# Kernel optimization log

Measured on AMD Instinct MI355X. Metric: run time of the kernel, lower is better.

The kernel has to match this reference:

```python
import math
import jax, jax.numpy as jnp
import numpy as np

D_MODEL = 1024
N_HEADS = 16


def setup_inputs() -> dict:
    key = jax.random.key(0)
    ks = jax.random.split(key, 5)
    B, S, D = 4, 2048, D_MODEL
    std = math.sqrt(2.0 / (D + D))
    x = jax.random.normal(ks[0], (B, S, D), dtype=jnp.float32)
    wq = jax.random.normal(ks[1], (D, D), dtype=jnp.float32) * std
    wk = jax.random.normal(ks[2], (D, D), dtype=jnp.float32) * std
    wv = jax.random.normal(ks[3], (D, D), dtype=jnp.float32) * std
    wo = jax.random.normal(ks[4], (D, D), dtype=jnp.float32) * std
    return {"x": x, "wq": wq, "wk": wk, "wv": wv, "wo": wo}


def reference(x, wq, wk, wv, wo):
    B, S, D = x.shape
    H = N_HEADS
    dk = D // H
    # projections: weight is (d_out, d_in) -> y_...j = x_...i W_ji
    def proj(w):
        y = jnp.einsum('bsi,ji->bsj', x, w)
        return y.reshape(B, S, H, dk).transpose(0, 2, 1, 3)  # b h s dk
    Q, K, V = proj(wq), proj(wk), proj(wv)
    scores = jnp.einsum('bhnd,bhmd->bhnm', Q, K) / math.sqrt(dk)
    causal = jnp.tril(jnp.ones((S, S), dtype=bool))  # True = attend
    scores = jnp.where(causal, scores, -jnp.inf)
    weights = jax.nn.softmax(scores, axis=-1)
    attn = jnp.einsum('bhnm,bhmd->bhnd', weights, V)
    attn = attn.transpose(0, 2, 1, 3).reshape(B, S, D)
    return jnp.einsum('bsi,ji->bsj', attn, wo)
```

## Files before the change

### kernel.cpp

```cpp
#include <hip/hip_runtime.h>
#include <hip/hip_bf16.h>
#include <cstdint>

#define D_MODEL 1024
#define NHEADS  16
#define DK      64
#define BATCH   4
#define SEQ     2048
#define MROWS   (BATCH * SEQ)
#define NQT2    (SEQ / 128)

#define QSCALE 0.18033688011112042f

typedef __attribute__((ext_vector_type(4))) float  f32x4;
typedef __attribute__((ext_vector_type(8))) __bf16 bf16x8;
typedef __attribute__((ext_vector_type(8))) short  short8;

__device__ __forceinline__ unsigned short f2bf(float f) {
    unsigned int u = __float_as_uint(f);
    unsigned int r = (u + 0x7fffu + ((u >> 16) & 1u)) >> 16;
    return (unsigned short)r;
}

__device__ __forceinline__ unsigned int cvtpk_bf16(float lo, float hi) {
    unsigned int r;
    asm volatile("v_cvt_pk_bf16_f32 %0, %1, %2" : "=v"(r) : "v"(lo), "v"(hi));
    return r;
}

__device__ __forceinline__ float exp2_raw(float x) {
    float r;
    asm("v_exp_f32 %0, %1" : "=v"(r) : "v"(x));
    return r;
}

__device__ __forceinline__ void permlane32_swap(unsigned int& a, unsigned int& b) {
    asm("v_permlane32_swap_b32 %0, %1" : "+v"(a), "+v"(b));
}
__device__ __forceinline__ void permlane16_swap(unsigned int& a, unsigned int& b) {
    asm("v_permlane16_swap_b32 %0, %1" : "+v"(a), "+v"(b));
}

__global__ void cvt_bf16(const float* __restrict__ in, unsigned short* __restrict__ out, int n) {
    int i = (blockIdx.x * 256 + threadIdx.x) * 4;
    if (i >= n) return;
    float4 v = *reinterpret_cast<const float4*>(in + i);
    ushort4 o;
    o.x = f2bf(v.x); o.y = f2bf(v.y); o.z = f2bf(v.z); o.w = f2bf(v.w);
    *reinterpret_cast<ushort4*>(out + i) = o;
}

__global__ void cvt_bf16_w(const float* __restrict__ w0, const float* __restrict__ w1,
                           const float* __restrict__ w2, const float* __restrict__ w3,
                           unsigned short* __restrict__ o0, unsigned short* __restrict__ o1,
                           unsigned short* __restrict__ o2, unsigned short* __restrict__ o3,
                           int n) {
    const int z = blockIdx.y;
    const float* in = (z == 0) ? w0 : (z == 1) ? w1 : (z == 2) ? w2 : w3;
    unsigned short* out = (z == 0) ? o0 : (z == 1) ? o1 : (z == 2) ? o2 : o3;
    int i = (blockIdx.x * 256 + threadIdx.x) * 4;
    if (i >= n) return;
    float4 v = *reinterpret_cast<const float4*>(in + i);
    ushort4 o;
    o.x = f2bf(v.x); o.y = f2bf(v.y); o.z = f2bf(v.z); o.w = f2bf(v.w);
    *reinterpret_cast<ushort4*>(out + i) = o;
}

__device__ __forceinline__ void gload_lds16(const void* g, void* l) {
    __builtin_amdgcn_global_load_lds(
        (const __attribute__((address_space(1))) void*)(uintptr_t)g,
        (__attribute__((address_space(3))) void*)(unsigned int)(uintptr_t)l,
        16, 0, 0);
}

#define BM 128
#define BN 128
#define BK 32

__global__ __launch_bounds__(256) void gemm_bt(
    const unsigned short* __restrict__ A,
    const unsigned short* __restrict__ B0,
    const unsigned short* __restrict__ B1,
    const unsigned short* __restrict__ B2,
    void* __restrict__ C0, void* __restrict__ C1, void* __restrict__ C2,
    int M, int N, int K, int out_f32, float scale_z0)
{
    __shared__ __align__(16) unsigned short As[2][BM * BK];
    __shared__ __align__(16) unsigned short Bs[2][BN * BK];

    const int z = blockIdx.z;
    const unsigned short* Bt = (z == 0) ? B0 : ((z == 1) ? B1 : B2);
    void* C = (z == 0) ? C0 : ((z == 1) ? C1 : C2);
    const float cs = (z == 0) ? scale_z0 : 1.0f;

    const int tid  = threadIdx.x;
    const int wave = tid >> 6;
    const int lane = tid & 63;
    const int wr   = wave >> 1;
    const int wc   = wave & 1;
    const int bm   = blockIdx.x * BM;
    const int bn   = blockIdx.y * BN;

    f32x4 acc[4][4];
    #pragma unroll
    for (int i = 0; i < 4; i++)
        #pragma unroll
        for (int j = 0; j < 4; j++)
            #pragma unroll
            for (int r = 0; r < 4; r++) acc[i][j][r] = 0.f;

    const int srow = tid >> 2;
    const int scol = (tid & 3) * 8;

    const int kg = (lane >> 4) * 8;
    const int rl = lane & 15;

    const unsigned short* Arow0 = A  + (size_t)(bm + srow) * K + scol;
    const unsigned short* Arow1 = A  + (size_t)(bm + 64 + srow) * K + scol;
    const unsigned short* Brow0 = Bt + (size_t)(bn + srow) * K + scol;
    const unsigned short* Brow1 = Bt + (size_t)(bn + 64 + srow) * K + scol;

    auto STAGE = [&](int buf, int k0) {
        gload_lds16(Arow0 + k0, &As[buf][0] + wave * 512);
        gload_lds16(Arow1 + k0, &As[buf][0] + 2048 + wave * 512);
        gload_lds16(Brow0 + k0, &Bs[buf][0] + wave * 512);
        gload_lds16(Brow1 + k0, &Bs[buf][0] + 2048 + wave * 512);
    };

    auto COMPUTE = [&](int buf) {
        bf16x8 a[4], b[4];
        #pragma unroll
        for (int mi = 0; mi < 4; mi++) {
            short8 t = *reinterpret_cast<const short8*>(&As[buf][(wr * 64 + mi * 16 + rl) * BK + kg]);
            a[mi] = __builtin_bit_cast(bf16x8, t);
        }
        #pragma unroll
        for (int ni = 0; ni < 4; ni++) {
            short8 t = *reinterpret_cast<const short8*>(&Bs[buf][(wc * 64 + ni * 16 + rl) * BK + kg]);
            b[ni] = __builtin_bit_cast(bf16x8, t);
        }
        #pragma unroll
        for (int mi = 0; mi < 4; mi++)
            #pragma unroll
            for (int ni = 0; ni < 4; ni++)
                acc[mi][ni] = __builtin_amdgcn_mfma_f32_16x16x32_bf16(a[mi], b[ni], acc[mi][ni], 0, 0, 0);
    };

    const int NT = K / BK;

    STAGE(0, 0);
    __syncthreads();

    int cur = 0;
    for (int t = 0; t < NT - 1; ++t) {
        STAGE(cur ^ 1, (t + 1) * BK);
        COMPUTE(cur);
        __syncthreads();
        cur ^= 1;
    }
    COMPUTE(cur);

    const int rg = (lane >> 4) * 4;
    if (out_f32) {
        #pragma unroll
        for (int mi = 0; mi < 4; mi++)
            #pragma unroll
            for (int ni = 0; ni < 4; ni++)
                #pragma unroll
                for (int r = 0; r < 4; r++) {
                    int row = bm + wr * 64 + mi * 16 + rg + r;
                    int col = bn + wc * 64 + ni * 16 + rl;
                    ((float*)C)[(size_t)row * N + col] = acc[mi][ni][r];
                }
    } else {
        #pragma unroll
        for (int mi = 0; mi < 4; mi++)
            #pragma unroll
            for (int ni = 0; ni < 4; ni++)
                #pragma unroll
                for (int r = 0; r < 4; r++) {
                    int row = bm + wr * 64 + mi * 16 + rg + r;
                    int col = bn + wc * 64 + ni * 16 + rl;
                    ((unsigned short*)C)[(size_t)row * N + col] = f2bf(acc[mi][ni][r] * cs);
                }
    }
}

__global__ __launch_bounds__(512, 4) void attn_mfma(
    const unsigned short* __restrict__ Q,
    const unsigned short* __restrict__ K,
    const unsigned short* __restrict__ V,
    unsigned short* __restrict__ O)
{
    __shared__ __align__(16) unsigned short Ks[2][64 * 64];
    __shared__ __align__(16) unsigned short Vt[2][64 * 64];

    const int bh  = blockIdx.x;
    const int b   = bh >> 4;
    const int h   = bh & 15;
    const int qt  = NQT2 - 1 - blockIdx.y;
    const int tid = threadIdx.x;
    const int wave = tid >> 6;
    const int lane = tid & 63;
    const int lg   = lane >> 4;
    const int lq   = lane & 15;

    const size_t base = ((size_t)b * SEQ) * D_MODEL + h * DK;
    const unsigned short* Kb = K + base;
    const unsigned short* Vb = V + base;

    const int qw  = qt * 128 + wave * 16;
    const int myq = qw + lq;

    bf16x8 qf[2];
    {
        const unsigned short* qp = Q + base + (size_t)myq * D_MODEL + lg * 8;
        qf[0] = __builtin_bit_cast(bf16x8, *reinterpret_cast<const short8*>(qp));
        qf[1] = __builtin_bit_cast(bf16x8, *reinterpret_cast<const short8*>(qp + 32));
    }

    const short8 ones_s = {(short)0x3F80, (short)0x3F80, (short)0x3F80, (short)0x3F80,
                           (short)0x3F80, (short)0x3F80, (short)0x3F80, (short)0x3F80};
    const bf16x8 onesf = __builtin_bit_cast(bf16x8, ones_s);

    f32x4 acc[4];
    f32x4 acc_l;
    #pragma unroll
    for (int i = 0; i < 4; i++)
        #pragma unroll
        for (int r = 0; r < 4; r++) acc[i][r] = 0.f;
    #pragma unroll
    for (int r = 0; r < 4; r++) acc_l[r] = 0.f;
    float m_run = -INFINITY;

    const int trow  = tid >> 3;
    const int tslot = tid & 7;
    const unsigned short* Ksrc = Kb + (size_t)trow * D_MODEL + (tslot ^ (trow & 7)) * 8;

    const unsigned short* Vsrc = Vb + (size_t)lane * D_MODEL + wave * 8;
    union { uint4 v; unsigned short u[8]; } vpre;

    const int nt = 2 * qt + 2;

    gload_lds16(Ksrc, &Ks[0][0] + wave * 512);
    vpre.v = *reinterpret_cast<const uint4*>(Vsrc);
    #pragma unroll
    for (int e = 0; e < 8; ++e) {
        const int addr = (wave * 8 + e) * 128 + ((lane * 2) ^ (e << 4));
        *reinterpret_cast<unsigned short*>((char*)&Vt[0][0] + addr) = vpre.u[e];
    }
    __syncthreads();

    for (int t = 0; t < nt; ++t) {
        const int c = t & 1;
        const bool pf = (t + 1 < nt);

        if (pf) {
            const size_t moff = (size_t)(t + 1) * 64 * D_MODEL;
            gload_lds16(Ksrc + moff, &Ks[c ^ 1][0] + wave * 512);
            vpre.v = *reinterpret_cast<const uint4*>(Vsrc + moff);
        }

        const int m0 = t * 64;

        if (m0 <= qw + 15) {
            f32x4 s[4];
            __builtin_amdgcn_s_setprio(1);
            #pragma unroll
            for (int kg = 0; kg < 4; ++kg) {
                #pragma unroll
                for (int r = 0; r < 4; ++r) s[kg][r] = 0.f;
                #pragma unroll
                for (int ks = 0; ks < 2; ++ks) {
                    const int row  = kg * 16 + lq;
                    const int slot = (ks * 4 + lg) ^ (row & 7);
                    bf16x8 kf = __builtin_bit_cast(bf16x8,
                        *reinterpret_cast<const short8*>((const char*)&Ks[c][0] + row * 128 + slot * 16));
                    s[kg] = __builtin_amdgcn_mfma_f32_16x16x32_bf16(kf, qf[ks], s[kg], 0, 0, 0);
                }
            }
            __builtin_amdgcn_s_setprio(0);

            if (m0 + 63 > qw) {
                #pragma unroll
                for (int kg = 0; kg < 4; ++kg)
                    #pragma unroll
                    for (int r = 0; r < 4; ++r)
                        if (m0 + kg * 16 + lg * 4 + r > myq) s[kg][r] = -INFINITY;
            }
            const float a0 = fmaxf(fmaxf(s[0][0], s[0][1]), fmaxf(s[0][2], s[0][3]));
            const float a1 = fmaxf(fmaxf(s[1][0], s[1][1]), fmaxf(s[1][2], s[1][3]));
            const float a2 = fmaxf(fmaxf(s[2][0], s[2][1]), fmaxf(s[2][2], s[2][3]));
            const float a3 = fmaxf(fmaxf(s[3][0], s[3][1]), fmaxf(s[3][2], s[3][3]));
            float mx = fmaxf(fmaxf(a0, a1), fmaxf(a2, a3));
            mx = fmaxf(mx, __shfl_xor(mx, 16));
            mx = fmaxf(mx, __shfl_xor(mx, 32));

            if (!__all(mx <= m_run + 12.f)) {
                const float mnew = fmaxf(m_run, mx);
                const float sc   = exp2_raw(m_run - mnew);
                m_run = mnew;
                float scv[4];
                #pragma unroll
                for (int r = 0; r < 4; ++r) scv[r] = __shfl(sc, lg * 4 + r);
                #pragma unroll
                for (int dg = 0; dg < 4; ++dg)
                    #pragma unroll
                    for (int r = 0; r < 4; ++r) acc[dg][r] *= scv[r];
                #pragma unroll
                for (int r = 0; r < 4; ++r) acc_l[r] *= scv[r];
            }

            float p[4][4];
            #pragma unroll
            for (int kg = 0; kg < 4; ++kg)
                #pragma unroll
                for (int r = 0; r < 4; ++r)
                    p[kg][r] = exp2_raw(s[kg][r] - m_run);

            #pragma unroll
            for (int ks = 0; ks < 2; ++ks) {
                unsigned int A0 = cvtpk_bf16(p[2*ks][0],   p[2*ks][1]);
                unsigned int A1 = cvtpk_bf16(p[2*ks][2],   p[2*ks][3]);
                unsigned int B0 = cvtpk_bf16(p[2*ks+1][0], p[2*ks+1][1]);
                unsigned int B1 = cvtpk_bf16(p[2*ks+1][2], p[2*ks+1][3]);
                permlane32_swap(A0, B0);
                permlane16_swap(A0, B0);
                permlane32_swap(A1, B1);
                permlane16_swap(A1, B1);
                uint4 awv = make_uint4(A0, A1, B0, B1);
                bf16x8 af = __builtin_bit_cast(bf16x8, awv);
                __builtin_amdgcn_s_setprio(1);
                #pragma unroll
                for (int dg = 0; dg < 4; ++dg) {
                    const int d = dg * 16 + lq;
                    const int addr = d * 128 + ((ks * 64 + lg * 16) ^ ((d & 7) << 4));
                    bf16x8 vf = __builtin_bit_cast(bf16x8,
                        *reinterpret_cast<const short8*>((const char*)&Vt[c][0] + addr));
                    acc[dg] = __builtin_amdgcn_mfma_f32_16x16x32_bf16(af, vf, acc[dg], 0, 0, 0);
                }
                acc_l = __builtin_amdgcn_mfma_f32_16x16x32_bf16(af, onesf, acc_l, 0, 0, 0);
                __builtin_amdgcn_s_setprio(0);
            }
        }

        if (pf) {
            #pragma unroll
            for (int e = 0; e < 8; ++e) {
                const int addr = (wave * 8 + e) * 128 + ((lane * 2) ^ (e << 4));
                *reinterpret_cast<unsigned short*>((char*)&Vt[c ^ 1][0] + addr) = vpre.u[e];
            }
        }
        __syncthreads();
    }

    float lv[4];
    #pragma unroll
    for (int r = 0; r < 4; ++r) lv[r] = 1.0f / acc_l[r];
    #pragma unroll
    for (int dg = 0; dg < 4; ++dg)
        #pragma unroll
        for (int r = 0; r < 4; ++r) {
            const int qrow = qw + lg * 4 + r;
            O[base + (size_t)qrow * D_MODEL + dg * 16 + lq] = f2bf(acc[dg][r] * lv[r]);
        }
}

extern "C" void kernel_launch(void* const* d_in, const int* in_sizes, int n_in,
                              void* d_out, int out_size, void* d_ws, size_t ws_size,
                              hipStream_t stream) {
    const float* x  = (const float*)d_in[0];
    const float* wq = (const float*)d_in[1];
    const float* wk = (const float*)d_in[2];
    const float* wv = (const float*)d_in[3];
    const float* wo = (const float*)d_in[4];

    char* ws = (char*)d_ws;
    const size_t NXB = (size_t)MROWS * D_MODEL * 2;
    const size_t NWB = (size_t)D_MODEL * D_MODEL * 2;

    unsigned short* xb  = (unsigned short*)(ws);
    unsigned short* wqb = (unsigned short*)(ws + NXB);
    unsigned short* wkb = (unsigned short*)(ws + NXB + NWB);
    unsigned short* wvb = (unsigned short*)(ws + NXB + 2 * NWB);
    unsigned short* wob = (unsigned short*)(ws + NXB + 3 * NWB);
    unsigned short* Qb  = (unsigned short*)(ws + NXB + 4 * NWB);
    unsigned short* Kb  = (unsigned short*)(ws + NXB + 4 * NWB + NXB);
    unsigned short* Vb  = (unsigned short*)(ws + NXB + 4 * NWB + 2 * NXB);
    unsigned short* Ab  = (unsigned short*)(ws + NXB + 4 * NWB + 3 * NXB);

    const int NX = MROWS * D_MODEL;
    const int NW = D_MODEL * D_MODEL;

    cvt_bf16<<<NX / 1024, 256, 0, stream>>>(x, xb, NX);
    dim3 gw(NW / 1024, 4, 1);
    cvt_bf16_w<<<gw, 256, 0, stream>>>(wq, wk, wv, wo, wqb, wkb, wvb, wob, NW);

    dim3 gqkv(MROWS / BM, D_MODEL / BN, 3);
    gemm_bt<<<gqkv, 256, 0, stream>>>(xb, wqb, wkb, wvb, Qb, Kb, Vb,
                                      MROWS, D_MODEL, D_MODEL, 0, QSCALE);

    dim3 gattn(BATCH * NHEADS, NQT2, 1);
    attn_mfma<<<gattn, 512, 0, stream>>>(Qb, Kb, Vb, Ab);

    dim3 gout(MROWS / BM, D_MODEL / BN, 1);
    gemm_bt<<<gout, 256, 0, stream>>>(Ab, wob, wob, wob, d_out, d_out, d_out,
                                      MROWS, D_MODEL, D_MODEL, 1, 1.0f);
}
```

Measured before the change: 179.7 us.

## Double the attention KV tile to 128 keys per iteration

Raises the attention kernel's K/V tile from 64 to 128 keys, so the loop runs half as many iterations, with half the barriers and online-softmax max/rescale steps. Each iteration loads two K chunks and two V vectors and computes eight score blocks. The causal mask is now applied only on the last tile and the per-wave skip of fully masked tiles is gone. That means waves whose queries sit early in the diagonal tile do some extra masked work. Shared memory per block doubles, which may reduce occupancy, and register pressure grows.

```diff
diff --git a/kernel.cpp b/kernel.cpp
--- a/kernel.cpp
+++ b/kernel.cpp
@@ -9,6 +9,7 @@
 #define SEQ     2048
 #define MROWS   (BATCH * SEQ)
 #define NQT2    (SEQ / 128)
+#define KVB     128
 
 #define QSCALE 0.18033688011112042f
 
@@ -192,8 +193,8 @@
     const unsigned short* __restrict__ V,
     unsigned short* __restrict__ O)
 {
-    __shared__ __align__(16) unsigned short Ks[2][64 * 64];
-    __shared__ __align__(16) unsigned short Vt[2][64 * 64];
+    __shared__ __align__(16) unsigned short Ks[2][KVB * 64];
+    __shared__ __align__(16) unsigned short Vt[2][64 * KVB];
 
     const int bh  = blockIdx.x;
     const int b   = bh >> 4;
@@ -235,20 +236,34 @@
 
     const int trow  = tid >> 3;
     const int tslot = tid & 7;
-    const unsigned short* Ksrc = Kb + (size_t)trow * D_MODEL + (tslot ^ (trow & 7)) * 8;
-
-    const unsigned short* Vsrc = Vb + (size_t)lane * D_MODEL + wave * 8;
-    union { uint4 v; unsigned short u[8]; } vpre;
-
-    const int nt = 2 * qt + 2;
-
-    gload_lds16(Ksrc, &Ks[0][0] + wave * 512);
-    vpre.v = *reinterpret_cast<const uint4*>(Vsrc);
-    #pragma unroll
-    for (int e = 0; e < 8; ++e) {
-        const int addr = (wave * 8 + e) * 128 + ((lane * 2) ^ (e << 4));
-        *reinterpret_cast<unsigned short*>((char*)&Vt[0][0] + addr) = vpre.u[e];
-    }
+    const int c0s = (tslot ^ (trow & 7)) * 8;
+    const unsigned short* Ksrc0 = Kb + (size_t)trow * D_MODEL + c0s;
+    const unsigned short* Ksrc1 = Kb + (size_t)(trow + 64) * D_MODEL + c0s;
+
+    const int vkey = tid & 127;
+    const int vd0  = (tid >> 7) * 8;
+    const unsigned short* Vsrc = Vb + (size_t)vkey * D_MODEL + vd0;
+    union { uint4 v; unsigned short u[8]; } vpre0, vpre1;
+
+    auto VWRITE = [&](int buf) {
+        #pragma unroll
+        for (int e = 0; e < 8; ++e) {
+            const int d = vd0 + e;
+            const int addr = d * 256 + ((vkey * 2) ^ ((d & 7) << 4));
+            *reinterpret_cast<unsigned short*>((char*)&Vt[buf][0] + addr) = vpre0.u[e];
+            const int d2 = d + 32;
+            const int addr2 = d2 * 256 + ((vkey * 2) ^ ((d2 & 7) << 4));
+            *reinterpret_cast<unsigned short*>((char*)&Vt[buf][0] + addr2) = vpre1.u[e];
+        }
+    };
+
+    const int nt = qt + 1;
+
+    gload_lds16(Ksrc0, &Ks[0][0] + wave * 512);
+    gload_lds16(Ksrc1, &Ks[0][0] + 4096 + wave * 512);
+    vpre0.v = *reinterpret_cast<const uint4*>(Vsrc);
+    vpre1.v = *reinterpret_cast<const uint4*>(Vsrc + 32);
+    VWRITE(0);
     __syncthreads();
 
     for (int t = 0; t < nt; ++t) {
@@ -256,101 +271,95 @@
         const bool pf = (t + 1 < nt);
 
         if (pf) {
-            const size_t moff = (size_t)(t + 1) * 64 * D_MODEL;
-            gload_lds16(Ksrc + moff, &Ks[c ^ 1][0] + wave * 512);
-            vpre.v = *reinterpret_cast<const uint4*>(Vsrc + moff);
-        }
-
-        const int m0 = t * 64;
-
-        if (m0 <= qw + 15) {
-            f32x4 s[4];
-            __builtin_amdgcn_s_setprio(1);
-            #pragma unroll
-            for (int kg = 0; kg < 4; ++kg) {
-                #pragma unroll
-                for (int r = 0; r < 4; ++r) s[kg][r] = 0.f;
-                #pragma unroll
-                for (int ks = 0; ks < 2; ++ks) {
-                    const int row  = kg * 16 + lq;
-                    const int slot = (ks * 4 + lg) ^ (row & 7);
-                    bf16x8 kf = __builtin_bit_cast(bf16x8,
-                        *reinterpret_cast<const short8*>((const char*)&Ks[c][0] + row * 128 + slot * 16));
-                    s[kg] = __builtin_amdgcn_mfma_f32_16x16x32_bf16(kf, qf[ks], s[kg], 0, 0, 0);
-                }
+            const size_t moff = (size_t)(t + 1) * KVB * D_MODEL;
+            gload_lds16(Ksrc0 + moff, &Ks[c ^ 1][0] + wave * 512);
+            gload_lds16(Ksrc1 + moff, &Ks[c ^ 1][0] + 4096 + wave * 512);
+            vpre0.v = *reinterpret_cast<const uint4*>(Vsrc + moff);
+            vpre1.v = *reinterpret_cast<const uint4*>(Vsrc + moff + 32);
+        }
+
+        const int m0 = t * KVB;
+
+        f32x4 s[8];
+        __builtin_amdgcn_s_setprio(1);
+        #pragma unroll
+        for (int kg = 0; kg < 8; ++kg) {
+            #pragma unroll
+            for (int r = 0; r < 4; ++r) s[kg][r] = 0.f;
+            #pragma unroll
+            for (int ks = 0; ks < 2; ++ks) {
+                const int row  = kg * 16 + lq;
+                const int slot = (ks * 4 + lg) ^ (row & 7);
+                bf16x8 kf = __builtin_bit_cast(bf16x8,
+                    *reinterpret_cast<const short8*>((const char*)&Ks[c][0] + row * 128 + slot * 16));
+                s[kg] = __builtin_amdgcn_mfma_f32_16x16x32_bf16(kf, qf[ks], s[kg], 0, 0, 0);
             }
-            __builtin_amdgcn_s_setprio(0);
-
-            if (m0 + 63 > qw) {
-                #pragma unroll
-                for (int kg = 0; kg < 4; ++kg)
-                    #pragma unroll
-                    for (int r = 0; r < 4; ++r)
-                        if (m0 + kg * 16 + lg * 4 + r > myq) s[kg][r] = -INFINITY;
-            }
-            const float a0 = fmaxf(fmaxf(s[0][0], s[0][1]), fmaxf(s[0][2], s[0][3]));
-            const float a1 = fmaxf(fmaxf(s[1][0], s[1][1]), fmaxf(s[1][2], s[1][3]));
-            const float a2 = fmaxf(fmaxf(s[2][0], s[2][1]), fmaxf(s[2][2], s[2][3]));
-            const float a3 = fmaxf(fmaxf(s[3][0], s[3][1]), fmaxf(s[3][2], s[3][3]));
-            float mx = fmaxf(fmaxf(a0, a1), fmaxf(a2, a3));
-            mx = fmaxf(mx, __shfl_xor(mx, 16));
-            mx = fmaxf(mx, __shfl_xor(mx, 32));
-
-            if (!__all(mx <= m_run + 12.f)) {
-                const float mnew = fmaxf(m_run, mx);
-                const float sc   = exp2_raw(m_run - mnew);
-                m_run = mnew;
-                float scv[4];
-                #pragma unroll
-                for (int r = 0; r < 4; ++r) scv[r] = __shfl(sc, lg * 4 + r);
-                #pragma unroll
-                for (int dg = 0; dg < 4; ++dg)
-                    #pragma unroll
-                    for (int r = 0; r < 4; ++r) acc[dg][r] *= scv[r];
-                #pragma unroll
-                for (int r = 0; r < 4; ++r) acc_l[r] *= scv[r];
-            }
-
-            float p[4][4];
-            #pragma unroll
-            for (int kg = 0; kg < 4; ++kg)
+        }
+        __builtin_amdgcn_s_setprio(0);
+
+        if (t == nt - 1) {
+            #pragma unroll
+            for (int kg = 0; kg < 8; ++kg)
                 #pragma unroll
                 for (int r = 0; r < 4; ++r)
-                    p[kg][r] = exp2_raw(s[kg][r] - m_run);
-
-            #pragma unroll
-            for (int ks = 0; ks < 2; ++ks) {
-                unsigned int A0 = cvtpk_bf16(p[2*ks][0],   p[2*ks][1]);
-                unsigned int A1 = cvtpk_bf16(p[2*ks][2],   p[2*ks][3]);
-                unsigned int B0 = cvtpk_bf16(p[2*ks+1][0], p[2*ks+1][1]);
-                unsigned int B1 = cvtpk_bf16(p[2*ks+1][2], p[2*ks+1][3]);
-                permlane32_swap(A0, B0);
-                permlane16_swap(A0, B0);
-                permlane32_swap(A1, B1);
-                permlane16_swap(A1, B1);
-                uint4 awv = make_uint4(A0, A1, B0, B1);
-                bf16x8 af = __builtin_bit_cast(bf16x8, awv);
-                __builtin_amdgcn_s_setprio(1);
+                    if (m0 + kg * 16 + lg * 4 + r > myq) s[kg][r] = -INFINITY;
+        }
+        float mk[8];
+        #pragma unroll
+        for (int kg = 0; kg < 8; ++kg)
+            mk[kg] = fmaxf(fmaxf(s[kg][0], s[kg][1]), fmaxf(s[kg][2], s[kg][3]));
+        float mx = fmaxf(fmaxf(fmaxf(mk[0], mk[1]), fmaxf(mk[2], mk[3])),
+                         fmaxf(fmaxf(mk[4], mk[5]), fmaxf(mk[6], mk[7])));
+        mx = fmaxf(mx, __shfl_xor(mx, 16));
+        mx = fmaxf(mx, __shfl_xor(mx, 32));
+
+        if (!__all(mx <= m_run + 12.f)) {
+            const float mnew = fmaxf(m_run, mx);
+            const float sc   = exp2_raw(m_run - mnew);
+            m_run = mnew;
+            float scv[4];
+            #pragma unroll
+            for (int r = 0; r < 4; ++r) scv[r] = __shfl(sc, lg * 4 + r);
+            #pragma unroll
+            for (int dg = 0; dg < 4; ++dg)
                 #pragma unroll
-                for (int dg = 0; dg < 4; ++dg) {
-                    const int d = dg * 16 + lq;
-                    const int addr = d * 128 + ((ks * 64 + lg * 16) ^ ((d & 7) << 4));
-                    bf16x8 vf = __builtin_bit_cast(bf16x8,
-                        *reinterpret_cast<const short8*>((const char*)&Vt[c][0] + addr));
-                    acc[dg] = __builtin_amdgcn_mfma_f32_16x16x32_bf16(af, vf, acc[dg], 0, 0, 0);
-                }
-                acc_l = __builtin_amdgcn_mfma_f32_16x16x32_bf16(af, onesf, acc_l, 0, 0, 0);
-                __builtin_amdgcn_s_setprio(0);
+                for (int r = 0; r < 4; ++r) acc[dg][r] *= scv[r];
+            #pragma unroll
+            for (int r = 0; r < 4; ++r) acc_l[r] *= scv[r];
+        }
+
+        #pragma unroll
+        for (int ksl = 0; ksl < 4; ++ksl) {
+            float p0[4], p1[4];
+            #pragma unroll
+            for (int r = 0; r < 4; ++r) {
+                p0[r] = exp2_raw(s[2*ksl][r]   - m_run);
+                p1[r] = exp2_raw(s[2*ksl+1][r] - m_run);
             }
-        }
-
-        if (pf) {
-            #pragma unroll
-            for (int e = 0; e < 8; ++e) {
-                const int addr = (wave * 8 + e) * 128 + ((lane * 2) ^ (e << 4));
-                *reinterpret_cast<unsigned short*>((char*)&Vt[c ^ 1][0] + addr) = vpre.u[e];
+            unsigned int A0 = cvtpk_bf16(p0[0], p0[1]);
+            unsigned int A1 = cvtpk_bf16(p0[2], p0[3]);
+            unsigned int B0 = cvtpk_bf16(p1[0], p1[1]);
+            unsigned int B1 = cvtpk_bf16(p1[2], p1[3]);
+            permlane32_swap(A0, B0);
+            permlane16_swap(A0, B0);
+            permlane32_swap(A1, B1);
+            permlane16_swap(A1, B1);
+            uint4 awv = make_uint4(A0, A1, B0, B1);
+            bf16x8 af = __builtin_bit_cast(bf16x8, awv);
+            __builtin_amdgcn_s_setprio(1);
+            #pragma unroll
+            for (int dg = 0; dg < 4; ++dg) {
+                const int d = dg * 16 + lq;
+                const int addr = d * 256 + ((ksl * 64 + lg * 16) ^ ((d & 7) << 4));
+                bf16x8 vf = __builtin_bit_cast(bf16x8,
+                    *reinterpret_cast<const short8*>((const char*)&Vt[c][0] + addr));
+                acc[dg] = __builtin_amdgcn_mfma_f32_16x16x32_bf16(af, vf, acc[dg], 0, 0, 0);
             }
-        }
+            acc_l = __builtin_amdgcn_mfma_f32_16x16x32_bf16(af, onesf, acc_l, 0, 0, 0);
+            __builtin_amdgcn_s_setprio(0);
+        }
+
+        if (pf) VWRITE(c ^ 1);
         __syncthreads();
     }
 
```

New measurement: 179.3 us. No clear change (-0.3%).

## Fuse Q/K/V projections into one GEMM sharing the A tile

Applied to the files above, without the earlier changes.

Replaces the z-indexed three-way QKV GEMM launch with a single kernel in which each block loads one x tile and three weight tiles, accumulating Q, K and V together (192 accumulator floats per lane). The x tile is read from global/LDS once instead of three times, and the grid shrinks from 1536 to 512 blocks. The cost is much higher register pressure and LDS use per block (launch bounds 256,2), which may lower occupancy or cause spills, and fewer blocks to spread across CUs. It relies on wq/wk/wv being contiguous in the workspace (W + w*NW_ELEM).

```diff
diff --git a/kernel.cpp b/kernel.cpp
--- a/kernel.cpp
+++ b/kernel.cpp
@@ -9,6 +9,7 @@
 #define SEQ     2048
 #define MROWS   (BATCH * SEQ)
 #define NQT2    (SEQ / 128)
+#define NW_ELEM (D_MODEL * D_MODEL)
 
 #define QSCALE 0.18033688011112042f
 
@@ -77,22 +78,17 @@
 #define BN 128
 #define BK 32
 
-__global__ __launch_bounds__(256) void gemm_bt(
+__global__ __launch_bounds__(256, 2) void gemm_qkv(
     const unsigned short* __restrict__ A,
-    const unsigned short* __restrict__ B0,
-    const unsigned short* __restrict__ B1,
-    const unsigned short* __restrict__ B2,
-    void* __restrict__ C0, void* __restrict__ C1, void* __restrict__ C2,
-    int M, int N, int K, int out_f32, float scale_z0)
+    const unsigned short* __restrict__ W,
+    unsigned short* __restrict__ Cq,
+    unsigned short* __restrict__ Ck,
+    unsigned short* __restrict__ Cv)
 {
     __shared__ __align__(16) unsigned short As[2][BM * BK];
-    __shared__ __align__(16) unsigned short Bs[2][BN * BK];
-
-    const int z = blockIdx.z;
-    const unsigned short* Bt = (z == 0) ? B0 : ((z == 1) ? B1 : B2);
-    void* C = (z == 0) ? C0 : ((z == 1) ? C1 : C2);
-    const float cs = (z == 0) ? scale_z0 : 1.0f;
-
+    __shared__ __align__(16) unsigned short Bs[3][2][BN * BK];
+
+    const int K = D_MODEL, N = D_MODEL;
     const int tid  = threadIdx.x;
     const int wave = tid >> 6;
     const int lane = tid & 63;
@@ -101,6 +97,105 @@
     const int bm   = blockIdx.x * BM;
     const int bn   = blockIdx.y * BN;
 
+    f32x4 acc[3][4][4];
+    #pragma unroll
+    for (int w = 0; w < 3; w++)
+        #pragma unroll
+        for (int i = 0; i < 4; i++)
+            #pragma unroll
+            for (int j = 0; j < 4; j++)
+                #pragma unroll
+                for (int r = 0; r < 4; r++) acc[w][i][j][r] = 0.f;
+
+    const int srow = tid >> 2;
+    const int scol = (tid & 3) * 8;
+
+    const int kg = (lane >> 4) * 8;
+    const int rl = lane & 15;
+
+    const unsigned short* Arow0 = A + (size_t)(bm + srow) * K + scol;
+    const unsigned short* Arow1 = A + (size_t)(bm + 64 + srow) * K + scol;
+    const unsigned short* Wrow0 = W + (size_t)(bn + srow) * K + scol;
+    const unsigned short* Wrow1 = W + (size_t)(bn + 64 + srow) * K + scol;
+
+    auto STAGE = [&](int buf, int k0) {
+        gload_lds16(Arow0 + k0, &As[buf][0] + wave * 512);
+        gload_lds16(Arow1 + k0, &As[buf][0] + 2048 + wave * 512);
+        #pragma unroll
+        for (int w = 0; w < 3; w++) {
+            gload_lds16(Wrow0 + (size_t)w * NW_ELEM + k0, &Bs[w][buf][0] + wave * 512);
+            gload_lds16(Wrow1 + (size_t)w * NW_ELEM + k0, &Bs[w][buf][0] + 2048 + wave * 512);
+        }
+    };
+
+    auto COMPUTE = [&](int buf) {
+        bf16x8 a[4];
+        #pragma unroll
+        for (int mi = 0; mi < 4; mi++) {
+            short8 t = *reinterpret_cast<const short8*>(&As[buf][(wr * 64 + mi * 16 + rl) * BK + kg]);
+            a[mi] = __builtin_bit_cast(bf16x8, t);
+        }
+        #pragma unroll
+        for (int w = 0; w < 3; w++)
+            #pragma unroll
+            for (int ni = 0; ni < 4; ni++) {
+                short8 t = *reinterpret_cast<const short8*>(&Bs[w][buf][(wc * 64 + ni * 16 + rl) * BK + kg]);
+                bf16x8 b = __builtin_bit_cast(bf16x8, t);
+                #pragma unroll
+                for (int mi = 0; mi < 4; mi++)
+                    acc[w][mi][ni] = __builtin_amdgcn_mfma_f32_16x16x32_bf16(a[mi], b, acc[w][mi][ni], 0, 0, 0);
+            }
+    };
+
+    const int NT = K / BK;
+
+    STAGE(0, 0);
+    __syncthreads();
+
+    int cur = 0;
+    for (int t = 0; t < NT - 1; ++t) {
+        STAGE(cur ^ 1, (t + 1) * BK);
+        COMPUTE(cur);
+        __syncthreads();
+        cur ^= 1;
+    }
+    COMPUTE(cur);
+
+    const int rg = (lane >> 4) * 4;
+    #pragma unroll
+    for (int w = 0; w < 3; w++) {
+        unsigned short* C = (w == 0) ? Cq : (w == 1) ? Ck : Cv;
+        const float cs = (w == 0) ? QSCALE : 1.0f;
+        #pragma unroll
+        for (int mi = 0; mi < 4; mi++)
+            #pragma unroll
+            for (int ni = 0; ni < 4; ni++)
+                #pragma unroll
+                for (int r = 0; r < 4; r++) {
+                    int row = bm + wr * 64 + mi * 16 + rg + r;
+                    int col = bn + wc * 64 + ni * 16 + rl;
+                    C[(size_t)row * N + col] = f2bf(acc[w][mi][ni][r] * cs);
+                }
+    }
+}
+
+__global__ __launch_bounds__(256) void gemm_out(
+    const unsigned short* __restrict__ A,
+    const unsigned short* __restrict__ Bt,
+    float* __restrict__ C)
+{
+    __shared__ __align__(16) unsigned short As[2][BM * BK];
+    __shared__ __align__(16) unsigned short Bs[2][BN * BK];
+
+    const int K = D_MODEL, N = D_MODEL;
+    const int tid  = threadIdx.x;
+    const int wave = tid >> 6;
+    const int lane = tid & 63;
+    const int wr   = wave >> 1;
+    const int wc   = wave & 1;
+    const int bm   = blockIdx.x * BM;
+    const int bn   = blockIdx.y * BN;
+
     f32x4 acc[4][4];
     #pragma unroll
     for (int i = 0; i < 4; i++)
@@ -161,29 +256,16 @@
     COMPUTE(cur);
 
     const int rg = (lane >> 4) * 4;
-    if (out_f32) {
-        #pragma unroll
-        for (int mi = 0; mi < 4; mi++)
-            #pragma unroll
-            for (int ni = 0; ni < 4; ni++)
-                #pragma unroll
-                for (int r = 0; r < 4; r++) {
-                    int row = bm + wr * 64 + mi * 16 + rg + r;
-                    int col = bn + wc * 64 + ni * 16 + rl;
-                    ((float*)C)[(size_t)row * N + col] = acc[mi][ni][r];
-                }
-    } else {
-        #pragma unroll
-        for (int mi = 0; mi < 4; mi++)
-            #pragma unroll
-            for (int ni = 0; ni < 4; ni++)
-                #pragma unroll
-                for (int r = 0; r < 4; r++) {
-                    int row = bm + wr * 64 + mi * 16 + rg + r;
-                    int col = bn + wc * 64 + ni * 16 + rl;
-                    ((unsigned short*)C)[(size_t)row * N + col] = f2bf(acc[mi][ni][r] * cs);
-                }
-    }
+    #pragma unroll
+    for (int mi = 0; mi < 4; mi++)
+        #pragma unroll
+        for (int ni = 0; ni < 4; ni++)
+            #pragma unroll
+            for (int r = 0; r < 4; r++) {
+                int row = bm + wr * 64 + mi * 16 + rg + r;
+                int col = bn + wc * 64 + ni * 16 + rl;
+                C[(size_t)row * N + col] = acc[mi][ni][r];
+            }
 }
 
 __global__ __launch_bounds__(512, 4) void attn_mfma(
@@ -396,14 +478,12 @@
     dim3 gw(NW / 1024, 4, 1);
     cvt_bf16_w<<<gw, 256, 0, stream>>>(wq, wk, wv, wo, wqb, wkb, wvb, wob, NW);
 
-    dim3 gqkv(MROWS / BM, D_MODEL / BN, 3);
-    gemm_bt<<<gqkv, 256, 0, stream>>>(xb, wqb, wkb, wvb, Qb, Kb, Vb,
-                                      MROWS, D_MODEL, D_MODEL, 0, QSCALE);
+    dim3 gqkv(MROWS / BM, D_MODEL / BN, 1);
+    gemm_qkv<<<gqkv, 256, 0, stream>>>(xb, wqb, Qb, Kb, Vb);
 
     dim3 gattn(BATCH * NHEADS, NQT2, 1);
     attn_mfma<<<gattn, 512, 0, stream>>>(Qb, Kb, Vb, Ab);
 
     dim3 gout(MROWS / BM, D_MODEL / BN, 1);
-    gemm_bt<<<gout, 256, 0, stream>>>(Ab, wob, wob, wob, d_out, d_out, d_out,
-                                      MROWS, D_MODEL, D_MODEL, 1, 1.0f);
-}
+    gemm_out<<<gout, 256, 0, stream>>>(Ab, wob, (float*)d_out);
+}
```

Measured after the change: 164.2 us. -8.6%, faster.
